# Performance work log

Hardware: AMD Instinct MI355X
Metric: run time of the kernel (lower is better)

## Reference

```python
import jax, jax.numpy as jnp
import numpy as np

B, S, DM, H = 4, 2048, 512, 8
HD = DM // H


def setup_inputs() -> dict:
    key = jax.random.key(0)
    ks = jax.random.split(key, 12)
    x = jax.random.normal(ks[0], (B, S, DM), dtype=jnp.float32)
    # causal lower-triangular mask [B, S, S]
    mask = jnp.broadcast_to(jnp.tril(jnp.ones((S, S), dtype=jnp.int32)), (B, S, S))
    # sorted irregular day offsets (trading-day-like), in days
    days_offset = jnp.sort(
        jax.random.uniform(ks[1], (B, S), dtype=jnp.float32) * 3000.0, axis=-1
    )
    scale = 1.0 / np.sqrt(DM)
    Wq = jax.random.normal(ks[2], (DM, DM), dtype=jnp.float32) * scale
    bq = jnp.zeros((DM,), dtype=jnp.float32)
    Wk = jax.random.normal(ks[3], (DM, DM), dtype=jnp.float32) * scale
    bk = jnp.zeros((DM,), dtype=jnp.float32)
    Wv = jax.random.normal(ks[4], (DM, DM), dtype=jnp.float32) * scale
    bv = jnp.zeros((DM,), dtype=jnp.float32)
    Wo = jax.random.normal(ks[5], (DM, DM), dtype=jnp.float32) * scale
    bo = jnp.zeros((DM,), dtype=jnp.float32)
    decay_rate = jnp.float32(0.1)
    return {
        "x": x, "mask": mask, "days_offset": days_offset,
        "Wq": Wq, "bq": bq, "Wk": Wk, "bk": bk,
        "Wv": Wv, "bv": bv, "Wo": Wo, "bo": bo,
        "decay_rate": decay_rate,
    }


def reference(x, mask, days_offset, Wq, bq, Wk, bk, Wv, bv, Wo, bo, decay_rate):
    b, s, _ = x.shape
    # projections (torch Linear: x @ W.T + b), split heads -> [b, h, s, hd]
    def proj(W, bias):
        return (x @ W.T + bias).reshape(b, s, H, HD).transpose(0, 2, 1, 3)
    q, k, v = proj(Wq, bq), proj(Wk, bk), proj(Wv, bv)
    scores = jnp.einsum("bhqd,bhkd->bhqk", q, k) / jnp.sqrt(jnp.float32(HD))
    # temporal decay: exp(-rate * |t_i - t_j|), broadcast over heads
    dist = jnp.abs(days_offset[:, :, None] - days_offset[:, None, :])  # [b,s,s]
    decay = jnp.exp(-decay_rate * dist)
    scores = scores * decay[:, None, :, :]
    scores = jnp.where(mask[:, None, :, :] == 0, -jnp.inf, scores)
    attn = jax.nn.softmax(scores, axis=-1)  # dropout p=0 (eval)
    out = jnp.einsum("bhqk,bhkd->bhqd", attn, v)
    out = out.transpose(0, 2, 1, 3).reshape(b, s, DM)
    return out @ Wo.T + bo
```

## Files before the change

kernel.cpp:

```cpp
#include <hip/hip_runtime.h>
#include <hip/hip_fp16.h>


#define S_LEN 2048
#define DMODEL 512
#define NH 8
#define HD 64

typedef _Float16 half8 __attribute__((ext_vector_type(8)));
typedef _Float16 half4 __attribute__((ext_vector_type(4)));
typedef float floatx4 __attribute__((ext_vector_type(4)));

__device__ __forceinline__ void gload16(const _Float16* g, _Float16* l) {
    __builtin_amdgcn_global_load_lds(
        (const __attribute__((address_space(1))) void*)g,
        (__attribute__((address_space(3))) void*)l, 16, 0, 0);
}

__device__ __forceinline__ half8 cvt8(float4 a, float4 b) {
    half8 h;
    h[0] = (_Float16)a.x; h[1] = (_Float16)a.y; h[2] = (_Float16)a.z; h[3] = (_Float16)a.w;
    h[4] = (_Float16)b.x; h[5] = (_Float16)b.y; h[6] = (_Float16)b.z; h[7] = (_Float16)b.w;
    return h;
}

__global__ __launch_bounds__(256) void qkv_gemm(
    const float* __restrict__ x,
    const float* __restrict__ Wq, const float* __restrict__ Wk, const float* __restrict__ Wv,
    const float* __restrict__ bq, const float* __restrict__ bk, const float* __restrict__ bv,
    _Float16* __restrict__ outh)
{
    __shared__ _Float16 As[128 * 64];
    __shared__ _Float16 Ws[128 * 64];
    const int t = threadIdx.x;
    const int bm = blockIdx.x, bn = blockIdx.y, z = blockIdx.z;
    const float* Wp = (z == 0) ? Wq : (z == 1) ? Wk : Wv;
    const float* bias = (z == 0) ? bq : (z == 1) ? bk : bv;
    const int w = t >> 6, lane = t & 63, l15 = lane & 15, quad = lane >> 4;
    const int wrow = (w >> 1) * 64, wcol = (w & 1) * 64;
    const int lrow = lane >> 3, lane7 = lane & 7;
    const int sw = lane7 ^ lrow;
    const float* xb = x  + (size_t)(bm * 128) * DMODEL;
    const float* Wb = Wp + (size_t)(bn * 128) * DMODEL;

    float4 pa[4][2], pw[4][2];
    auto ldf = [&](int kb) {
        #pragma unroll
        for (int i = 0; i < 4; ++i) {
            const float* p = xb + (size_t)(w * 32 + i * 8 + lrow) * DMODEL + kb * 64 + sw * 8;
            pa[i][0] = *(const float4*)p; pa[i][1] = *(const float4*)(p + 4);
            const float* q = Wb + (size_t)(w * 32 + i * 8 + lrow) * DMODEL + kb * 64 + sw * 8;
            pw[i][0] = *(const float4*)q; pw[i][1] = *(const float4*)(q + 4);
        }
    };

    floatx4 acc[4][4] = {};
    ldf(0);
    for (int kb = 0; kb < 8; ++kb) {
        __syncthreads();
        #pragma unroll
        for (int i = 0; i < 4; ++i) {
            int row = w * 32 + i * 8 + lrow;
            *(half8*)(&As[row * 64 + lane7 * 8]) = cvt8(pa[i][0], pa[i][1]);
            *(half8*)(&Ws[row * 64 + lane7 * 8]) = cvt8(pw[i][0], pw[i][1]);
        }
        __syncthreads();
        if (kb < 7) ldf(kb + 1);
        #pragma unroll
        for (int kk = 0; kk < 2; ++kk) {
            half8 xf[4], wf[4];
            #pragma unroll
            for (int mt = 0; mt < 4; ++mt)
                xf[mt] = *(const half8*)(&As[(wrow + mt * 16 + l15) * 64 + (((quad + 4 * kk) ^ (l15 & 7)) * 8)]);
            #pragma unroll
            for (int nt = 0; nt < 4; ++nt)
                wf[nt] = *(const half8*)(&Ws[(wcol + nt * 16 + l15) * 64 + (((quad + 4 * kk) ^ (l15 & 7)) * 8)]);
            if (z == 2) {
                #pragma unroll
                for (int mt = 0; mt < 4; ++mt)
                    #pragma unroll
                    for (int nt = 0; nt < 4; ++nt)
                        acc[mt][nt] = __builtin_amdgcn_mfma_f32_16x16x32_f16(xf[mt], wf[nt], acc[mt][nt], 0, 0, 0);
            } else {
                #pragma unroll
                for (int nt = 0; nt < 4; ++nt)
                    #pragma unroll
                    for (int mt = 0; mt < 4; ++mt)
                        acc[nt][mt] = __builtin_amdgcn_mfma_f32_16x16x32_f16(wf[nt], xf[mt], acc[nt][mt], 0, 0, 0);
            }
        }
    }

    if (z == 2) {
        #pragma unroll
        for (int mt = 0; mt < 4; ++mt)
            #pragma unroll
            for (int nt = 0; nt < 4; ++nt) {
                int n = bn * 128 + wcol + nt * 16 + l15;
                float bvv = bias[n];
                int m0 = bm * 128 + wrow + mt * 16 + quad * 4;
                int b = m0 >> 11, s0 = m0 & 2047;
                int hh = n >> 6, hd = n & 63;
                half4 hv;
                #pragma unroll
                for (int r = 0; r < 4; ++r) hv[r] = (_Float16)(acc[mt][nt][r] + bvv);
                *(half4*)(outh + (size_t)2 * (8192 * 512) +
                          ((size_t)(b * NH + hh) * HD + hd) * S_LEN + s0) = hv;
            }
    } else {
        #pragma unroll
        for (int nt = 0; nt < 4; ++nt)
            #pragma unroll
            for (int mt = 0; mt < 4; ++mt) {
                int n0 = bn * 128 + wcol + nt * 16 + quad * 4;
                float4 b4 = *(const float4*)(bias + n0);
                int m = bm * 128 + wrow + mt * 16 + l15;
                int b = m >> 11, s = m & 2047;
                int hh = n0 >> 6, hd0 = n0 & 63;
                half4 hv;
                hv[0] = (_Float16)(acc[nt][mt][0] + b4.x);
                hv[1] = (_Float16)(acc[nt][mt][1] + b4.y);
                hv[2] = (_Float16)(acc[nt][mt][2] + b4.z);
                hv[3] = (_Float16)(acc[nt][mt][3] + b4.w);
                *(half4*)(outh + (size_t)z * (8192 * 512) +
                          ((size_t)(b * NH + hh) * S_LEN + s) * HD + hd0) = hv;
            }
    }
}

__global__ __launch_bounds__(256) void out_gemm(
    const _Float16* __restrict__ A, const float* __restrict__ Wo,
    const float* __restrict__ bo, float* __restrict__ outf)
{
    __shared__ _Float16 As[64 * 64];
    __shared__ _Float16 Ws[128 * 64];
    const int t = threadIdx.x;
    const int bm = blockIdx.x, bn = blockIdx.y;
    const int w = t >> 6, lane = t & 63, l15 = lane & 15, quad = lane >> 4;
    const int wn = w * 32;
    const int lrow = lane >> 3, lane7 = lane & 7;
    const int sw = lane7 ^ lrow;
    const _Float16* Ab = A  + (size_t)(bm * 64) * DMODEL;
    const float*    Wb = Wo + (size_t)(bn * 128) * DMODEL;

    half8 pa[2];
    float4 pw[4][2];
    auto ldf = [&](int kb) {
        #pragma unroll
        for (int i = 0; i < 2; ++i)
            pa[i] = *(const half8*)(Ab + (size_t)((w * 2 + i) * 8 + lrow) * DMODEL + kb * 64 + sw * 8);
        #pragma unroll
        for (int i = 0; i < 4; ++i) {
            const float* q = Wb + (size_t)(w * 32 + i * 8 + lrow) * DMODEL + kb * 64 + sw * 8;
            pw[i][0] = *(const float4*)q; pw[i][1] = *(const float4*)(q + 4);
        }
    };

    floatx4 acc[2][4] = {};
    ldf(0);
    for (int kb = 0; kb < 8; ++kb) {
        __syncthreads();
        #pragma unroll
        for (int i = 0; i < 2; ++i)
            *(half8*)(&As[((w * 2 + i) * 8 + lrow) * 64 + lane7 * 8]) = pa[i];
        #pragma unroll
        for (int i = 0; i < 4; ++i)
            *(half8*)(&Ws[(w * 32 + i * 8 + lrow) * 64 + lane7 * 8]) = cvt8(pw[i][0], pw[i][1]);
        __syncthreads();
        if (kb < 7) ldf(kb + 1);
        #pragma unroll
        for (int kk = 0; kk < 2; ++kk) {
            half8 wf[2], af[4];
            #pragma unroll
            for (int nt = 0; nt < 2; ++nt)
                wf[nt] = *(const half8*)(&Ws[(wn + nt * 16 + l15) * 64 + (((quad + 4 * kk) ^ (l15 & 7)) * 8)]);
            #pragma unroll
            for (int mt = 0; mt < 4; ++mt)
                af[mt] = *(const half8*)(&As[(mt * 16 + l15) * 64 + (((quad + 4 * kk) ^ (l15 & 7)) * 8)]);
            #pragma unroll
            for (int nt = 0; nt < 2; ++nt)
                #pragma unroll
                for (int mt = 0; mt < 4; ++mt)
                    acc[nt][mt] = __builtin_amdgcn_mfma_f32_16x16x32_f16(wf[nt], af[mt], acc[nt][mt], 0, 0, 0);
        }
    }

    #pragma unroll
    for (int nt = 0; nt < 2; ++nt)
        #pragma unroll
        for (int mt = 0; mt < 4; ++mt) {
            int n0 = bn * 128 + wn + nt * 16 + quad * 4;
            float4 b4 = *(const float4*)(bo + n0);
            int m = bm * 64 + mt * 16 + l15;
            float4 v;
            v.x = acc[nt][mt][0] + b4.x; v.y = acc[nt][mt][1] + b4.y;
            v.z = acc[nt][mt][2] + b4.z; v.w = acc[nt][mt][3] + b4.w;
            *(float4*)(outf + (size_t)m * DMODEL + n0) = v;
        }
}

__global__ __launch_bounds__(256, 2) void attn_k(
    const _Float16* __restrict__ Qh, const _Float16* __restrict__ Kh,
    const _Float16* __restrict__ Vt, const float* __restrict__ days,
    const float* __restrict__ rate_p, _Float16* __restrict__ Ah)
{
    __shared__ _Float16 Ks[2][64 * 64];
    __shared__ _Float16 Vs[2][64 * 64];
    __shared__ float    eks[2][64];
    __shared__ _Float16 Ps[4][16 * 64];

    const int h = blockIdx.x, pr = blockIdx.y, b = blockIdx.z;
    const int t = threadIdx.x, w = t >> 6, lane = t & 63, l15 = lane & 15, quad = lane >> 4;
    const float rate = rate_p[0];
    const size_t bhoff = (size_t)(b * NH + h) * (size_t)(S_LEN * HD);
    const _Float16* Qb = Qh + bhoff;
    const _Float16* Kb = Kh + bhoff;
    const _Float16* Vb = Vt + bhoff;
    const float* daysb = days + b * S_LEN;
    const int lrow = lane >> 3, sw = (lane & 7) ^ lrow;
    const int e7 = l15 & 7;

    auto stage = [&](int kt, int buf) {
        #pragma unroll
        for (int i = 0; i < 2; ++i) {
            int grp = w * 2 + i;
            int row = grp * 8 + lrow;
            gload16(Kb + (size_t)(kt * 64 + row) * HD + sw * 8, &Ks[buf][grp * 512]);
            gload16(Vb + (size_t)row * S_LEN + kt * 64 + sw * 8, &Vs[buf][grp * 512]);
        }
        if (w == 0) {
            float tk0 = daysb[kt * 64];
            float d = daysb[kt * 64 + lane];
            eks[buf][lane] = __expf(fminf(rate * (d - tk0), 80.f));
        }
    };

    auto run_phase = [&](int j, int par0, int nextj) -> int {
        const int qg = j * 64 + w * 16 + l15;
        half8 qf0 = *(const half8*)(Qb + (size_t)qg * HD + quad * 8);
        half8 qf1 = *(const half8*)(Qb + (size_t)qg * HD + 32 + quad * 8);
        const float tq = daysb[qg];
        floatx4 oacc[4] = {};
        float lacc = 0.f;

        for (int kt = 0; kt <= j; ++kt) {
            const int par = (par0 + kt) & 1;
            __syncthreads();
            if (kt < j) stage(kt + 1, par ^ 1);
            else if (nextj >= 0) stage(0, par ^ 1);
            const float tk0 = daysb[kt * 64];
            half8 kf[4][2];
            #pragma unroll
            for (int c = 0; c < 4; ++c)
                #pragma unroll
                for (int kk = 0; kk < 2; ++kk)
                    kf[c][kk] = *(const half8*)(&Ks[par][(c * 16 + l15) * 64 + (((quad + 4 * kk) ^ e7) * 8)]);
            floatx4 sc[4];
            #pragma unroll
            for (int c = 0; c < 4; ++c) {
                floatx4 z4 = {};
                z4 = __builtin_amdgcn_mfma_f32_16x16x32_f16(kf[c][0], qf0, z4, 0, 0, 0);
                sc[c] = __builtin_amdgcn_mfma_f32_16x16x32_f16(kf[c][1], qf1, z4, 0, 0, 0);
            }
            half8 vf[4][2];
            #pragma unroll
            for (int s4 = 0; s4 < 4; ++s4)
                #pragma unroll
                for (int kk = 0; kk < 2; ++kk)
                    vf[s4][kk] = *(const half8*)(&Vs[par][(s4 * 16 + l15) * 64 + (((quad + 4 * kk) ^ e7) * 8)]);
            floatx4 ekv[4];
            #pragma unroll
            for (int c = 0; c < 4; ++c)
                ekv[c] = *(const floatx4*)(&eks[par][c * 16 + quad * 4]);
            const float eq = 0.125f * __expf(-rate * (tq - tk0));
            const bool dg = (kt == j);
            #pragma unroll
            for (int c = 0; c < 4; ++c) {
                float pvv[4];
                #pragma unroll
                for (int r = 0; r < 4; ++r) {
                    float sv = sc[c][r] * (eq * ekv[c][r]);
                    float p = __expf(sv - 2.0f);
                    if (dg && (kt * 64 + c * 16 + quad * 4 + r) > qg) p = 0.f;
                    lacc += p;
                    pvv[r] = p;
                }
                half4 hv;
                hv.x = (_Float16)pvv[0]; hv.y = (_Float16)pvv[1];
                hv.z = (_Float16)pvv[2]; hv.w = (_Float16)pvv[3];
                *(half4*)(&Ps[w][l15 * 64 + (((2 * c + (quad >> 1)) ^ e7) * 8) + (quad & 1) * 4]) = hv;
            }
            half8 pf0 = *(const half8*)(&Ps[w][l15 * 64 + ((quad ^ e7) * 8)]);
            half8 pf1 = *(const half8*)(&Ps[w][l15 * 64 + (((4 + quad) ^ e7) * 8)]);
            #pragma unroll
            for (int s4 = 0; s4 < 4; ++s4) {
                oacc[s4] = __builtin_amdgcn_mfma_f32_16x16x32_f16(vf[s4][0], pf0, oacc[s4], 0, 0, 0);
                oacc[s4] = __builtin_amdgcn_mfma_f32_16x16x32_f16(vf[s4][1], pf1, oacc[s4], 0, 0, 0);
            }
        }

        float l = lacc;
        l += __shfl_xor(l, 16);
        l += __shfl_xor(l, 32);
        float linv = 1.0f / l;
        #pragma unroll
        for (int s4 = 0; s4 < 4; ++s4) {
            half4 hv;
            #pragma unroll
            for (int r = 0; r < 4; ++r) hv[r] = (_Float16)(oacc[s4][r] * linv);
            *(half4*)(Ah + ((size_t)(b * S_LEN) + qg) * DMODEL + h * HD + s4 * 16 + quad * 4) = hv;
        }
        return (par0 + j + 1) & 1;
    };

    const int j0 = pr, j1 = 31 - pr;
    stage(0, 0);
    int p1 = run_phase(j0, 0, j1);
    run_phase(j1, p1, -1);
}

extern "C" void kernel_launch(void* const* d_in, const int* in_sizes, int n_in,
                              void* d_out, int out_size, void* d_ws, size_t ws_size,
                              hipStream_t stream)
{
    const float* x    = (const float*)d_in[0];
    const float* days = (const float*)d_in[2];
    const float* Wq   = (const float*)d_in[3];
    const float* bq   = (const float*)d_in[4];
    const float* Wk   = (const float*)d_in[5];
    const float* bk   = (const float*)d_in[6];
    const float* Wv   = (const float*)d_in[7];
    const float* bv   = (const float*)d_in[8];
    const float* Wo   = (const float*)d_in[9];
    const float* bo   = (const float*)d_in[10];
    const float* rate = (const float*)d_in[11];
    float* out = (float*)d_out;

    _Float16* Qh = (_Float16*)d_ws;
    _Float16* Kh = Qh + 4194304;
    _Float16* Vh = Kh + 4194304;
    _Float16* Ah = Vh + 4194304;

    dim3 g0(64, 4, 3);
    qkv_gemm<<<g0, 256, 0, stream>>>(x, Wq, Wk, Wv, bq, bk, bv, Qh);

    dim3 ga(NH, 16, 4);
    attn_k<<<ga, 256, 0, stream>>>(Qh, Kh, Vh, days, rate, Ah);

    dim3 g1(128, 4, 1);
    out_gemm<<<g1, 256, 0, stream>>>(Ah, Wo, bo, out);
}
```

Baseline: 213.2 us.

## Double-buffer GEMM LDS tiles, load direct-to-LDS, split diagonal softmax path

Both projection GEMMs now use two LDS buffers with one barrier per K step instead of two. The next tile is staged into the other buffer while the current one feeds the MFMAs, and out_gemm loads its fp16 A tile straight into LDS with global_load_lds. In the attention loop, the diagonal causal tile gets its own branch so off-diagonal tiles skip the mask test, and the constant -2 exponent shift is removed. In exchange, LDS use doubles, which may lower occupancy. The fp32 loads now sit directly before their LDS stores rather than being prefetched into registers, so less global latency may be hidden.

```diff
diff --git a/kernel.cpp b/kernel.cpp
--- a/kernel.cpp
+++ b/kernel.cpp
@@ -24,14 +24,24 @@
     return h;
 }
 
+__device__ __forceinline__ void stage_f32(
+    const float* __restrict__ src, _Float16* __restrict__ dstbase,
+    int row, int sw, int lane7, int kcol)
+{
+    const float* p = src + (size_t)row * DMODEL + kcol + sw * 8;
+    float4 a = *(const float4*)p;
+    float4 b = *(const float4*)(p + 4);
+    *(half8*)(dstbase + row * 64 + lane7 * 8) = cvt8(a, b);
+}
+
 __global__ __launch_bounds__(256) void qkv_gemm(
     const float* __restrict__ x,
     const float* __restrict__ Wq, const float* __restrict__ Wk, const float* __restrict__ Wv,
     const float* __restrict__ bq, const float* __restrict__ bk, const float* __restrict__ bv,
     _Float16* __restrict__ outh)
 {
-    __shared__ _Float16 As[128 * 64];
-    __shared__ _Float16 Ws[128 * 64];
+    __shared__ _Float16 As[2][128 * 64];
+    __shared__ _Float16 Ws[2][128 * 64];
     const int t = threadIdx.x;
     const int bm = blockIdx.x, bn = blockIdx.y, z = blockIdx.z;
     const float* Wp = (z == 0) ? Wq : (z == 1) ? Wk : Wv;
@@ -43,38 +53,30 @@
     const float* xb = x  + (size_t)(bm * 128) * DMODEL;
     const float* Wb = Wp + (size_t)(bn * 128) * DMODEL;
 
-    float4 pa[4][2], pw[4][2];
-    auto ldf = [&](int kb) {
-        #pragma unroll
-        for (int i = 0; i < 4; ++i) {
-            const float* p = xb + (size_t)(w * 32 + i * 8 + lrow) * DMODEL + kb * 64 + sw * 8;
-            pa[i][0] = *(const float4*)p; pa[i][1] = *(const float4*)(p + 4);
-            const float* q = Wb + (size_t)(w * 32 + i * 8 + lrow) * DMODEL + kb * 64 + sw * 8;
-            pw[i][0] = *(const float4*)q; pw[i][1] = *(const float4*)(q + 4);
-        }
-    };
-
-    floatx4 acc[4][4] = {};
-    ldf(0);
-    for (int kb = 0; kb < 8; ++kb) {
-        __syncthreads();
+    auto stage = [&](int kb, int buf) {
         #pragma unroll
         for (int i = 0; i < 4; ++i) {
             int row = w * 32 + i * 8 + lrow;
-            *(half8*)(&As[row * 64 + lane7 * 8]) = cvt8(pa[i][0], pa[i][1]);
-            *(half8*)(&Ws[row * 64 + lane7 * 8]) = cvt8(pw[i][0], pw[i][1]);
-        }
+            stage_f32(xb, As[buf], row, sw, lane7, kb * 64);
+            stage_f32(Wb, Ws[buf], row, sw, lane7, kb * 64);
+        }
+    };
+
+    floatx4 acc[4][4] = {};
+    stage(0, 0);
+    for (int kb = 0; kb < 8; ++kb) {
+        const int buf = kb & 1;
         __syncthreads();
-        if (kb < 7) ldf(kb + 1);
+        if (kb < 7) stage(kb + 1, buf ^ 1);
         #pragma unroll
         for (int kk = 0; kk < 2; ++kk) {
             half8 xf[4], wf[4];
             #pragma unroll
             for (int mt = 0; mt < 4; ++mt)
-                xf[mt] = *(const half8*)(&As[(wrow + mt * 16 + l15) * 64 + (((quad + 4 * kk) ^ (l15 & 7)) * 8)]);
+                xf[mt] = *(const half8*)(&As[buf][(wrow + mt * 16 + l15) * 64 + (((quad + 4 * kk) ^ (l15 & 7)) * 8)]);
             #pragma unroll
             for (int nt = 0; nt < 4; ++nt)
-                wf[nt] = *(const half8*)(&Ws[(wcol + nt * 16 + l15) * 64 + (((quad + 4 * kk) ^ (l15 & 7)) * 8)]);
+                wf[nt] = *(const half8*)(&Ws[buf][(wcol + nt * 16 + l15) * 64 + (((quad + 4 * kk) ^ (l15 & 7)) * 8)]);
             if (z == 2) {
                 #pragma unroll
                 for (int mt = 0; mt < 4; ++mt)
@@ -132,8 +134,8 @@
     const _Float16* __restrict__ A, const float* __restrict__ Wo,
     const float* __restrict__ bo, float* __restrict__ outf)
 {
-    __shared__ _Float16 As[64 * 64];
-    __shared__ _Float16 Ws[128 * 64];
+    __shared__ _Float16 As[2][64 * 64];
+    __shared__ _Float16 Ws[2][128 * 64];
     const int t = threadIdx.x;
     const int bm = blockIdx.x, bn = blockIdx.y;
     const int w = t >> 6, lane = t & 63, l15 = lane & 15, quad = lane >> 4;
@@ -143,40 +145,32 @@
     const _Float16* Ab = A  + (size_t)(bm * 64) * DMODEL;
     const float*    Wb = Wo + (size_t)(bn * 128) * DMODEL;
 
-    half8 pa[2];
-    float4 pw[4][2];
-    auto ldf = [&](int kb) {
-        #pragma unroll
-        for (int i = 0; i < 2; ++i)
-            pa[i] = *(const half8*)(Ab + (size_t)((w * 2 + i) * 8 + lrow) * DMODEL + kb * 64 + sw * 8);
-        #pragma unroll
-        for (int i = 0; i < 4; ++i) {
-            const float* q = Wb + (size_t)(w * 32 + i * 8 + lrow) * DMODEL + kb * 64 + sw * 8;
-            pw[i][0] = *(const float4*)q; pw[i][1] = *(const float4*)(q + 4);
-        }
+    auto stage = [&](int kb, int buf) {
+        #pragma unroll
+        for (int i = 0; i < 2; ++i) {
+            int row = (w * 2 + i) * 8 + lrow;
+            gload16(Ab + (size_t)row * DMODEL + kb * 64 + sw * 8, &As[buf][row * 64]);
+        }
+        #pragma unroll
+        for (int i = 0; i < 4; ++i)
+            stage_f32(Wb, Ws[buf], w * 32 + i * 8 + lrow, sw, lane7, kb * 64);
     };
 
     floatx4 acc[2][4] = {};
-    ldf(0);
+    stage(0, 0);
     for (int kb = 0; kb < 8; ++kb) {
+        const int buf = kb & 1;
         __syncthreads();
-        #pragma unroll
-        for (int i = 0; i < 2; ++i)
-            *(half8*)(&As[((w * 2 + i) * 8 + lrow) * 64 + lane7 * 8]) = pa[i];
-        #pragma unroll
-        for (int i = 0; i < 4; ++i)
-            *(half8*)(&Ws[(w * 32 + i * 8 + lrow) * 64 + lane7 * 8]) = cvt8(pw[i][0], pw[i][1]);
-        __syncthreads();
-        if (kb < 7) ldf(kb + 1);
+        if (kb < 7) stage(kb + 1, buf ^ 1);
         #pragma unroll
         for (int kk = 0; kk < 2; ++kk) {
             half8 wf[2], af[4];
             #pragma unroll
             for (int nt = 0; nt < 2; ++nt)
-                wf[nt] = *(const half8*)(&Ws[(wn + nt * 16 + l15) * 64 + (((quad + 4 * kk) ^ (l15 & 7)) * 8)]);
+                wf[nt] = *(const half8*)(&Ws[buf][(wn + nt * 16 + l15) * 64 + (((quad + 4 * kk) ^ (l15 & 7)) * 8)]);
             #pragma unroll
             for (int mt = 0; mt < 4; ++mt)
-                af[mt] = *(const half8*)(&As[(mt * 16 + l15) * 64 + (((quad + 4 * kk) ^ (l15 & 7)) * 8)]);
+                af[mt] = *(const half8*)(&As[buf][(mt * 16 + l15) * 64 + (((quad + 4 * kk) ^ (l15 & 7)) * 8)]);
             #pragma unroll
             for (int nt = 0; nt < 2; ++nt)
                 #pragma unroll
@@ -268,27 +262,42 @@
                 #pragma unroll
                 for (int kk = 0; kk < 2; ++kk)
                     vf[s4][kk] = *(const half8*)(&Vs[par][(s4 * 16 + l15) * 64 + (((quad + 4 * kk) ^ e7) * 8)]);
-            floatx4 ekv[4];
+            const float eq = 0.125f * __expf(-rate * (tq - tk0));
+            floatx4 eqk[4];
             #pragma unroll
             for (int c = 0; c < 4; ++c)
-                ekv[c] = *(const floatx4*)(&eks[par][c * 16 + quad * 4]);
-            const float eq = 0.125f * __expf(-rate * (tq - tk0));
-            const bool dg = (kt == j);
-            #pragma unroll
-            for (int c = 0; c < 4; ++c) {
-                float pvv[4];
-                #pragma unroll
-                for (int r = 0; r < 4; ++r) {
-                    float sv = sc[c][r] * (eq * ekv[c][r]);
-                    float p = __expf(sv - 2.0f);
-                    if (dg && (kt * 64 + c * 16 + quad * 4 + r) > qg) p = 0.f;
-                    lacc += p;
-                    pvv[r] = p;
+                eqk[c] = eq * *(const floatx4*)(&eks[par][c * 16 + quad * 4]);
+            if (kt == j) {
+                #pragma unroll
+                for (int c = 0; c < 4; ++c) {
+                    float pvv[4];
+                    #pragma unroll
+                    for (int r = 0; r < 4; ++r) {
+                        float p = __expf(sc[c][r] * eqk[c][r]);
+                        if ((kt * 64 + c * 16 + quad * 4 + r) > qg) p = 0.f;
+                        lacc += p;
+                        pvv[r] = p;
+                    }
+                    half4 hv;
+                    hv[0] = (_Float16)pvv[0]; hv[1] = (_Float16)pvv[1];
+                    hv[2] = (_Float16)pvv[2]; hv[3] = (_Float16)pvv[3];
+                    *(half4*)(&Ps[w][l15 * 64 + (((2 * c + (quad >> 1)) ^ e7) * 8) + (quad & 1) * 4]) = hv;
                 }
-                half4 hv;
-                hv.x = (_Float16)pvv[0]; hv.y = (_Float16)pvv[1];
-                hv.z = (_Float16)pvv[2]; hv.w = (_Float16)pvv[3];
-                *(half4*)(&Ps[w][l15 * 64 + (((2 * c + (quad >> 1)) ^ e7) * 8) + (quad & 1) * 4]) = hv;
+            } else {
+                #pragma unroll
+                for (int c = 0; c < 4; ++c) {
+                    float pvv[4];
+                    #pragma unroll
+                    for (int r = 0; r < 4; ++r) {
+                        float p = __expf(sc[c][r] * eqk[c][r]);
+                        lacc += p;
+                        pvv[r] = p;
+                    }
+                    half4 hv;
+                    hv[0] = (_Float16)pvv[0]; hv[1] = (_Float16)pvv[1];
+                    hv[2] = (_Float16)pvv[2]; hv[3] = (_Float16)pvv[3];
+                    *(half4*)(&Ps[w][l15 * 64 + (((2 * c + (quad >> 1)) ^ e7) * 8) + (quad & 1) * 4]) = hv;
+                }
             }
             half8 pf0 = *(const half8*)(&Ps[w][l15 * 64 + ((quad ^ e7) * 8)]);
             half8 pf1 = *(const half8*)(&Ps[w][l15 * 64 + (((4 + quad) ^ e7) * 8)]);
```

After: 207.3 us. 1.03x faster.
